# Optimization experiments

Hardware: AMD Instinct MI355X
Metric: run time of the kernel (lower is better)

Reference implementation:

```python
import jax, jax.numpy as jnp
import numpy as np
from jax import lax

B, C, H, W = 32, 128, 56, 56
SIZE = C * H * W
EPS = 1e-5
SLOPE = 0.1


def setup_inputs() -> dict:
    key = jax.random.key(0)
    ks = jax.random.split(key, 12)
    return {
        "ax": jax.random.normal(ks[0], (B, C, H, W), dtype=jnp.float32),
        "mx": jax.random.normal(ks[1], (B, C, H, W), dtype=jnp.float32),
        # grouped conv1d (groups=SIZE, k=2, no bias) == per-position pair weights [SIZE, 2]
        "cfc_w": jax.random.normal(ks[2], (SIZE, 2), dtype=jnp.float32) * 0.1,
        # BatchNorm1d (eval mode) params over SIZE channels
        "bn_gamma": jax.random.normal(ks[3], (SIZE,), dtype=jnp.float32) * 0.1 + 1.0,
        "bn_beta": jax.random.normal(ks[4], (SIZE,), dtype=jnp.float32) * 0.1,
        "bn_mean": jax.random.normal(ks[5], (SIZE,), dtype=jnp.float32) * 0.1,
        "bn_var": jax.random.uniform(ks[6], (SIZE,), dtype=jnp.float32, minval=0.5, maxval=1.5),
        # conv3x3, C->C, bias
        "conv_w": jax.random.normal(ks[7], (C, C, 3, 3), dtype=jnp.float32) * (1.0 / np.sqrt(C * 9)),
        "conv_b": jax.random.normal(ks[8], (C,), dtype=jnp.float32) * 0.01,
        # BatchNorm2d (eval mode) params over C channels
        "bn2_gamma": jax.random.normal(ks[9], (C,), dtype=jnp.float32) * 0.1 + 1.0,
        "bn2_beta": jax.random.normal(ks[10], (C,), dtype=jnp.float32) * 0.1,
        "bn2_mean": jax.random.normal(ks[11], (C,), dtype=jnp.float32) * 0.1,
        "bn2_var": jax.random.uniform(jax.random.fold_in(key, 99), (C,), dtype=jnp.float32, minval=0.5, maxval=1.5),
    }


def reference(ax, mx, cfc_w, bn_gamma, bn_beta, bn_mean, bn_var,
              conv_w, conv_b, bn2_gamma, bn2_beta, bn2_mean, bn2_var):
    b, c, h, w = ax.shape
    a = ax.reshape(b, -1)  # [B, SIZE]
    m = mx.reshape(b, -1)
    # degenerate grouped Conv1d(k=2, groups=SIZE): z_i = w_i0 * a_i + w_i1 * m_i
    z = cfc_w[:, 0] * a + cfc_w[:, 1] * m
    # BatchNorm1d (eval) + LeakyReLU(0.1)
    z = (z - bn_mean) * (bn_gamma / jnp.sqrt(bn_var + EPS)) + bn_beta
    z = jax.nn.leaky_relu(z, SLOPE).reshape(b, c, h, w)
    # conv3x3 (stride 1, pad 1) + bias
    y = lax.conv_general_dilated(z, conv_w, window_strides=(1, 1),
                                 padding=((1, 1), (1, 1)),
                                 dimension_numbers=("NCHW", "OIHW", "NCHW"))
    y = y + conv_b[None, :, None, None]
    # BatchNorm2d (eval) + LeakyReLU(0.1)
    scale = (bn2_gamma / jnp.sqrt(bn2_var + EPS))[None, :, None, None]
    y = (y - bn2_mean[None, :, None, None]) * scale + bn2_beta[None, :, None, None]
    return jax.nn.leaky_relu(y, SLOPE)
```

## Files before the change

### kernel.cpp

```cpp
#include <hip/hip_runtime.h>

#define B_ 32
#define C_ 128
#define H_ 56
#define W_ 56
#define HW_ (H_*W_)
#define SIZE_ (C_*HW_)
#define NPIX_ (B_*HW_)
#define HP_ 58
#define WP_ 58
#define PLANE_ (HP_*WP_*C_)
#define K_ 1152
#define EPS_ 1e-5f
#define SLOPE_ 0.1f

typedef __bf16 bf16x8 __attribute__((ext_vector_type(8)));
typedef float  f32x4  __attribute__((ext_vector_type(4)));

__device__ __forceinline__ ushort f2bf(float x) {
    union { float f; unsigned u; } v; v.f = x;
    return (ushort)((v.u + 0x7FFFu + ((v.u >> 16) & 1u)) >> 16);
}
__device__ __forceinline__ float lrelu(float z) { return z > 0.f ? z : SLOPE_ * z; }

__device__ __forceinline__ void glds16(const ushort* g, ushort* l) {
    __builtin_amdgcn_global_load_lds(
        (const __attribute__((address_space(1))) unsigned int*)g,
        (__attribute__((address_space(3))) unsigned int*)l, 16, 0, 0);
}

__global__ __launch_bounds__(256) void prep_kernel(
    const float* __restrict__ conv_w, const float* __restrict__ conv_b,
    const float* __restrict__ g2, const float* __restrict__ b2,
    const float* __restrict__ m2, const float* __restrict__ v2,
    const float2* __restrict__ cfc, const float* __restrict__ g1,
    const float* __restrict__ b1, const float* __restrict__ mu1,
    const float* __restrict__ v1,
    ushort* __restrict__ wA, float* __restrict__ scale2, float* __restrict__ shift2,
    float* __restrict__ p0, float* __restrict__ p1, float* __restrict__ p2)
{
    int tid = blockIdx.x * 256 + threadIdx.x;
    if (tid < C_ * K_) {
        int co = tid / K_;
        int k  = tid - co * K_;
        int khkw = k >> 7, ci = k & 127;
        int kh = khkw / 3, kw = khkw - 3 * kh;
        wA[tid] = f2bf(conv_w[((co * C_ + ci) * 3 + kh) * 3 + kw]);
    }
    if (tid < C_) {
        float sc = g2[tid] * rsqrtf(v2[tid] + EPS_);
        scale2[tid] = sc;
        shift2[tid] = (conv_b[tid] - m2[tid]) * sc + b2[tid];
    }
    if (tid < SIZE_) {
        float sc = g1[tid] * rsqrtf(v1[tid] + EPS_);
        float2 wv = cfc[tid];
        p0[tid] = wv.x * sc;
        p1[tid] = wv.y * sc;
        p2[tid] = b1[tid] - mu1[tid] * sc;
    }
}

__global__ __launch_bounds__(256) void zfuse_kernel(
    const float4* __restrict__ ax, const float4* __restrict__ mx,
    const float4* __restrict__ p0, const float4* __restrict__ p1,
    const float4* __restrict__ p2, ushort* __restrict__ zp)
{
    __shared__ ushort tile[W_ * 132];
    const int hp = blockIdx.x, b = blockIdx.y;
    const int tid = threadIdx.x;
    ushort* row = zp + (size_t)b * PLANE_ + (size_t)hp * (WP_ * C_);
    if (hp == 0 || hp == HP_ - 1) {
        uint2* r2 = (uint2*)row;
        for (int i = tid; i < WP_ * C_ / 4; i += 256) r2[i] = make_uint2(0u, 0u);
        return;
    }
    const int h = hp - 1;
    const int base4 = (b * SIZE_) >> 2;
    for (int i = tid; i < 1792; i += 256) {
        int c  = i / 14;
        int w4 = i - c * 14;
        int s4 = c * (HW_ / 4) + h * (W_ / 4) + w4;
        float4 a = ax[base4 + s4];
        float4 m = mx[base4 + s4];
        float4 q0 = p0[s4], q1 = p1[s4], q2 = p2[s4];
        int wb = w4 * 4;
        tile[(wb + 0) * 132 + c] = f2bf(lrelu(a.x * q0.x + m.x * q1.x + q2.x));
        tile[(wb + 1) * 132 + c] = f2bf(lrelu(a.y * q0.y + m.y * q1.y + q2.y));
        tile[(wb + 2) * 132 + c] = f2bf(lrelu(a.z * q0.z + m.z * q1.z + q2.z));
        tile[(wb + 3) * 132 + c] = f2bf(lrelu(a.w * q0.w + m.w * q1.w + q2.w));
    }
    __syncthreads();
    if (tid < C_) {
        row[tid] = 0;
        row[(WP_ - 1) * C_ + tid] = 0;
    }
    for (int j = tid; j < 1792; j += 256) {
        int w = j >> 5, cc = j & 31;
        *(uint2*)(row + C_ + w * C_ + cc * 4) = *(const uint2*)(tile + w * 132 + cc * 4);
    }
}

__global__ __launch_bounds__(256, 3) void conv_kernel(
    const ushort* __restrict__ zp, const ushort* __restrict__ wA,
    const float* __restrict__ scale2, const float* __restrict__ shift2,
    float* __restrict__ out)
{
    __shared__ ushort As[3][128 * 32];
    __shared__ ushort Bs[3][128 * 32];

    const int tid  = threadIdx.x;
    const int wave = tid >> 6, lane = tid & 63;
    const int l16  = lane & 15, quad = lane >> 4;
    const int pbase = blockIdx.x * 128;

    const int srow = wave * 32 + (lane >> 2);
    const int skey = (srow >> 1) & 3;
    const int sch  = (lane & 3) ^ skey;
    const ushort* agA = wA + srow * K_ + sch * 8;

    int pf0 = pbase + srow;
    int bb0 = pf0 / HW_, pi0 = pf0 - bb0 * HW_;
    int h0 = pi0 / W_, w0 = pi0 - h0 * W_;
    const ushort* bgB0 = zp + (size_t)bb0 * PLANE_ + (h0 * WP_ + w0) * C_ + sch * 8;
    int pf1 = pf0 + 16;
    int bb1 = pf1 / HW_, pi1 = pf1 - bb1 * HW_;
    int h1 = pi1 / W_, w1 = pi1 - h1 * W_;
    const ushort* bgB1 = zp + (size_t)bb1 * PLANE_ + (h1 * WP_ + w1) * C_ + sch * 8;

    const int lofs0 = (wave * 32) * 32;
    const int lofs1 = (wave * 32 + 16) * 32;

    const int cob = (wave & 1) * 64;
    const int pxb = (wave >> 1) * 64;
    const int rquad = quad ^ ((l16 >> 1) & 3);

    f32x4 acc[4][4] = {};

#define STAGE(buf, aoff, boff)                                    \
    do {                                                          \
        glds16(agA + (aoff),           As[buf] + lofs0);          \
        glds16(agA + 16 * K_ + (aoff), As[buf] + lofs1);          \
        glds16(bgB0 + (boff),          Bs[buf] + lofs0);          \
        glds16(bgB1 + (boff),          Bs[buf] + lofs1);          \
    } while (0)

#define BOFF(t) ((((t) >> 2) / 3 * WP_ + ((t) >> 2) % 3) * C_ + ((t) & 3) * 32)

    STAGE(0, 0, BOFF(0));
    STAGE(1, 32, BOFF(1));

    #pragma unroll
    for (int t = 0; t < 36; ++t) {
        if (t < 35) asm volatile("s_waitcnt vmcnt(4)" ::: "memory");
        else        asm volatile("s_waitcnt vmcnt(0)" ::: "memory");
        __builtin_amdgcn_s_barrier();
        __builtin_amdgcn_sched_barrier(0);
        if (t <= 33) {
            const int t2 = t + 2;
            STAGE(t2 % 3, t2 * 32, BOFF(t2));
        }
        const int buf = t % 3;
        bf16x8 af[4], bfr[4];
        #pragma unroll
        for (int mt = 0; mt < 4; ++mt)
            af[mt] = *(const bf16x8*)(As[buf] + (cob + mt * 16 + l16) * 32 + rquad * 8);
        #pragma unroll
        for (int nt = 0; nt < 4; ++nt)
            bfr[nt] = *(const bf16x8*)(Bs[buf] + (pxb + nt * 16 + l16) * 32 + rquad * 8);
        #pragma unroll
        for (int mt = 0; mt < 4; ++mt)
            #pragma unroll
            for (int nt = 0; nt < 4; ++nt)
                acc[mt][nt] = __builtin_amdgcn_mfma_f32_16x16x32_bf16(
                    af[mt], bfr[nt], acc[mt][nt], 0, 0, 0);
    }
#undef STAGE
#undef BOFF

    int pob[4];
    #pragma unroll
    for (int nt = 0; nt < 4; ++nt) {
        int pf = pbase + pxb + nt * 16 + l16;
        int bb = pf / HW_;
        pob[nt] = bb * SIZE_ + (pf - bb * HW_);
    }
    #pragma unroll
    for (int mt = 0; mt < 4; ++mt) {
        #pragma unroll
        for (int r = 0; r < 4; ++r) {
            int co = cob + mt * 16 + quad * 4 + r;
            float sc = scale2[co], sh = shift2[co];
            #pragma unroll
            for (int nt = 0; nt < 4; ++nt) {
                float v = acc[mt][nt][r] * sc + sh;
                out[(size_t)pob[nt] + co * HW_] = lrelu(v);
            }
        }
    }
}

extern "C" void kernel_launch(void* const* d_in, const int* in_sizes, int n_in,
                              void* d_out, int out_size, void* d_ws, size_t ws_size,
                              hipStream_t stream) {
    const float* ax     = (const float*)d_in[0];
    const float* mx     = (const float*)d_in[1];
    const float* cfc    = (const float*)d_in[2];
    const float* bn_g   = (const float*)d_in[3];
    const float* bn_b   = (const float*)d_in[4];
    const float* bn_m   = (const float*)d_in[5];
    const float* bn_v   = (const float*)d_in[6];
    const float* conv_w = (const float*)d_in[7];
    const float* conv_b = (const float*)d_in[8];
    const float* g2     = (const float*)d_in[9];
    const float* b2     = (const float*)d_in[10];
    const float* m2     = (const float*)d_in[11];
    const float* v2     = (const float*)d_in[12];
    float* out = (float*)d_out;

    char* ws = (char*)d_ws;
    ushort* zp     = (ushort*)ws;
    ushort* wA     = (ushort*)(ws + 27557888);
    float*  scale2 = (float*)(ws + 27852800);
    float*  shift2 = (float*)(ws + 27853312);
    float*  p0     = (float*)(ws + 27853824);
    float*  p1     = (float*)(ws + 29459456);
    float*  p2     = (float*)(ws + 31065088);

    prep_kernel<<<dim3((SIZE_ + 255) / 256), 256, 0, stream>>>(
        conv_w, conv_b, g2, b2, m2, v2, (const float2*)cfc,
        bn_g, bn_b, bn_m, bn_v, wA, scale2, shift2, p0, p1, p2);
    zfuse_kernel<<<dim3(HP_, B_), 256, 0, stream>>>(
        (const float4*)ax, (const float4*)mx,
        (const float4*)p0, (const float4*)p1, (const float4*)p2, zp);
    conv_kernel<<<dim3(NPIX_ / 128), 256, 0, stream>>>(zp, wA, scale2, shift2, out);
}
```

Measured before the change: 241.8 us.

## Split padded activations and weights into 32-channel K-slab planes, swizzle block order

The padded bf16 activation buffer changes from NHWC with 128 channels per pixel to four separate planes of 32 channels each, and the conv weights are reordered so every 32-wide K step is a contiguous 128x32 block. With this layout each pipeline stage's global-to-LDS loads read contiguous 64-byte rows instead of strided slices of 256-byte pixel records. The conv grid is also remapped so neighbouring block IDs fall in different regions of the pixel range, which changes how work is distributed and cached across the GPU. The risk is more scattered writes in the fused z kernel and worse locality if the block remapping spreads out data reuse.

Measured after the change: 237.2 us. Within noise of the previous version (-1.9%).

```diff
diff --git a/kernel.cpp b/kernel.cpp
--- a/kernel.cpp
+++ b/kernel.cpp
@@ -9,7 +9,7 @@
 #define NPIX_ (B_*HW_)
 #define HP_ 58
 #define WP_ 58
-#define PLANE_ (HP_*WP_*C_)
+#define PLSZ_ (B_*HP_*WP_*32)
 #define K_ 1152
 #define EPS_ 1e-5f
 #define SLOPE_ 0.1f
@@ -43,9 +43,10 @@
     if (tid < C_ * K_) {
         int co = tid / K_;
         int k  = tid - co * K_;
+        int t  = k >> 5, kk = k & 31;
         int khkw = k >> 7, ci = k & 127;
         int kh = khkw / 3, kw = khkw - 3 * kh;
-        wA[tid] = f2bf(conv_w[((co * C_ + ci) * 3 + kh) * 3 + kw]);
+        wA[(t * C_ + co) * 32 + kk] = f2bf(conv_w[((co * C_ + ci) * 3 + kh) * 3 + kw]);
     }
     if (tid < C_) {
         float sc = g2[tid] * rsqrtf(v2[tid] + EPS_);
@@ -69,10 +70,12 @@
     __shared__ ushort tile[W_ * 132];
     const int hp = blockIdx.x, b = blockIdx.y;
     const int tid = threadIdx.x;
-    ushort* row = zp + (size_t)b * PLANE_ + (size_t)hp * (WP_ * C_);
+    const int rb = (b * HP_ + hp) * (WP_ * 32);
     if (hp == 0 || hp == HP_ - 1) {
-        uint2* r2 = (uint2*)row;
-        for (int i = tid; i < WP_ * C_ / 4; i += 256) r2[i] = make_uint2(0u, 0u);
+        for (int ks = 0; ks < 4; ++ks) {
+            uint2* r2 = (uint2*)(zp + ks * PLSZ_ + rb);
+            for (int i = tid; i < WP_ * 32 / 4; i += 256) r2[i] = make_uint2(0u, 0u);
+        }
         return;
     }
     const int h = hp - 1;
@@ -91,13 +94,15 @@
         tile[(wb + 3) * 132 + c] = f2bf(lrelu(a.w * q0.w + m.w * q1.w + q2.w));
     }
     __syncthreads();
-    if (tid < C_) {
-        row[tid] = 0;
-        row[(WP_ - 1) * C_ + tid] = 0;
+    {
+        int side = (tid >> 7) & 1, ks = (tid >> 5) & 3, cc = tid & 31;
+        zp[ks * PLSZ_ + rb + (side ? (WP_ - 1) * 32 : 0) + cc] = 0;
     }
     for (int j = tid; j < 1792; j += 256) {
-        int w = j >> 5, cc = j & 31;
-        *(uint2*)(row + C_ + w * C_ + cc * 4) = *(const uint2*)(tile + w * 132 + cc * 4);
+        int ks = j / 448, r = j - ks * 448;
+        int w = r >> 3, cc = r & 7;
+        *(uint2*)(zp + ks * PLSZ_ + rb + (w + 1) * 32 + cc * 4) =
+            *(const uint2*)(tile + w * 132 + ks * 32 + cc * 4);
     }
 }
 
@@ -112,21 +117,22 @@
     const int tid  = threadIdx.x;
     const int wave = tid >> 6, lane = tid & 63;
     const int l16  = lane & 15, quad = lane >> 4;
-    const int pbase = blockIdx.x * 128;
+    const int bid  = blockIdx.x;
+    const int pbase = ((bid & 7) * 98 + (bid >> 3)) * 128;
 
     const int srow = wave * 32 + (lane >> 2);
     const int skey = (srow >> 1) & 3;
     const int sch  = (lane & 3) ^ skey;
-    const ushort* agA = wA + srow * K_ + sch * 8;
+    const ushort* agA = wA + srow * 32 + sch * 8;
 
     int pf0 = pbase + srow;
     int bb0 = pf0 / HW_, pi0 = pf0 - bb0 * HW_;
     int h0 = pi0 / W_, w0 = pi0 - h0 * W_;
-    const ushort* bgB0 = zp + (size_t)bb0 * PLANE_ + (h0 * WP_ + w0) * C_ + sch * 8;
+    const ushort* bgB0 = zp + ((bb0 * HP_ + h0) * WP_ + w0) * 32 + sch * 8;
     int pf1 = pf0 + 16;
     int bb1 = pf1 / HW_, pi1 = pf1 - bb1 * HW_;
     int h1 = pi1 / W_, w1 = pi1 - h1 * W_;
-    const ushort* bgB1 = zp + (size_t)bb1 * PLANE_ + (h1 * WP_ + w1) * C_ + sch * 8;
+    const ushort* bgB1 = zp + ((bb1 * HP_ + h1) * WP_ + w1) * 32 + sch * 8;
 
     const int lofs0 = (wave * 32) * 32;
     const int lofs1 = (wave * 32 + 16) * 32;
@@ -137,18 +143,18 @@
 
     f32x4 acc[4][4] = {};
 
-#define STAGE(buf, aoff, boff)                                    \
-    do {                                                          \
-        glds16(agA + (aoff),           As[buf] + lofs0);          \
-        glds16(agA + 16 * K_ + (aoff), As[buf] + lofs1);          \
-        glds16(bgB0 + (boff),          Bs[buf] + lofs0);          \
-        glds16(bgB1 + (boff),          Bs[buf] + lofs1);          \
+#define STAGE(buf, t)                                                      \
+    do {                                                                   \
+        glds16(agA + (t) * 4096,        As[buf] + lofs0);                  \
+        glds16(agA + (t) * 4096 + 512,  As[buf] + lofs1);                  \
+        glds16(bgB0 + BOFF(t),          Bs[buf] + lofs0);                  \
+        glds16(bgB1 + BOFF(t),          Bs[buf] + lofs1);                  \
     } while (0)
 
-#define BOFF(t) ((((t) >> 2) / 3 * WP_ + ((t) >> 2) % 3) * C_ + ((t) & 3) * 32)
-
-    STAGE(0, 0, BOFF(0));
-    STAGE(1, 32, BOFF(1));
+#define BOFF(t) (((t) & 3) * PLSZ_ + (((((t) >> 2) / 3) * WP_ + (((t) >> 2) % 3)) * 32))
+
+    STAGE(0, 0);
+    STAGE(1, 1);
 
     #pragma unroll
     for (int t = 0; t < 36; ++t) {
@@ -157,8 +163,7 @@
         __builtin_amdgcn_s_barrier();
         __builtin_amdgcn_sched_barrier(0);
         if (t <= 33) {
-            const int t2 = t + 2;
-            STAGE(t2 % 3, t2 * 32, BOFF(t2));
+            STAGE((t + 2) % 3, t + 2);
         }
         const int buf = t % 3;
         bf16x8 af[4], bfr[4];
```
